# Performance work log

Measured on AMD Instinct MI355X. Metric: run time of the kernel, lower is better.

The kernel has to match this reference:

```python
import jax, jax.numpy as jnp
import numpy as np

N_NODES = 100000
N_EDGES = 1600000
HIDDEN = 128
HALF = HIDDEN // 2
LN_EPS = 1e-5


def setup_inputs() -> dict:
    key = jax.random.key(0)
    ks = jax.random.split(key, 8)
    pos = jax.random.normal(ks[0], (N_NODES, 3), dtype=jnp.float32) * 10.0
    edge_index = jax.random.randint(ks[1], (2, N_EDGES), 0, N_NODES, dtype=jnp.int64)
    batch = jnp.zeros((N_NODES,), dtype=jnp.int64)
    # spatial_encoder params: Linear(3, HALF) -> LayerNorm(HALF) -> GELU -> Linear(HALF, HALF)
    W1 = jax.random.normal(ks[2], (3, HALF), dtype=jnp.float32) * 0.3
    b1 = jax.random.normal(ks[3], (HALF,), dtype=jnp.float32) * 0.05
    ln_g = jnp.ones((HALF,), dtype=jnp.float32)
    ln_b = jnp.zeros((HALF,), dtype=jnp.float32)
    W2 = jax.random.normal(ks[4], (HALF, HALF), dtype=jnp.float32) * 0.1
    b2 = jax.random.normal(ks[5], (HALF,), dtype=jnp.float32) * 0.05
    return {"pos": pos, "edge_index": edge_index, "batch": batch,
            "W1": W1, "b1": b1, "ln_g": ln_g, "ln_b": ln_b, "W2": W2, "b2": b2}


def _layernorm(x, g, b):
    mu = jnp.mean(x, axis=-1, keepdims=True)
    var = jnp.mean((x - mu) ** 2, axis=-1, keepdims=True)
    return (x - mu) * jax.lax.rsqrt(var + LN_EPS) * g + b


def reference(pos, edge_index, batch, W1, b1, ln_g, ln_b, W2, b2):
    num_nodes = pos.shape[0]
    src, dst = edge_index[0], edge_index[1]
    rel = pos[dst] - pos[src]                              # [E, 3]
    dist = jnp.linalg.norm(rel, axis=1, keepdims=True)     # [E, 1]
    rel_n = rel / (dist + 1e-6)
    h = rel_n @ W1 + b1                                    # [E, HALF]
    h = _layernorm(h, ln_g, ln_b)
    h = jax.nn.gelu(h, approximate=False)                  # torch exact GELU
    code = h @ W2 + b2                                     # dropout is identity in eval
    agg = jax.ops.segment_sum(code, dst, num_segments=num_nodes)          # [N, HALF]
    deg = jax.ops.segment_sum(jnp.ones_like(dst, dtype=code.dtype), dst,
                              num_segments=num_nodes)
    deg = jnp.clip(deg, 1.0)
    agg = agg / deg[:, None]
    # original buffer is [N, HIDDEN]; only the first HALF channels receive updates
    out = jnp.concatenate([agg, jnp.zeros_like(agg)], axis=1)             # [N, HIDDEN]
    return out
```

## Files before the change

### kernel.cpp

```cpp
#include <hip/hip_runtime.h>
#include <math.h>

#define HALF 64
#define LN_EPS 1e-5f
#define TCAP 1024
#define TSTR 16

#define GC0 -2.3022082f
#define GC1 -0.1029438f

typedef float f32x2 __attribute__((ext_vector_type(2)));

__device__ __forceinline__ f32x2 pk_fma(f32x2 a, f32x2 b, f32x2 c) {
    f32x2 d;
    asm("v_pk_fma_f32 %0, %1, %2, %3" : "=v"(d) : "v"(a), "v"(b), "v"(c));
    return d;
}
__device__ __forceinline__ f32x2 pk_mul(f32x2 a, f32x2 b) {
    f32x2 d;
    asm("v_pk_mul_f32 %0, %1, %2" : "=v"(d) : "v"(a), "v"(b));
    return d;
}

__device__ __forceinline__ float gelu_fast(float x) {
    const float x2 = x * x;
    const float z  = x * fmaf(GC1, x2, GC0);
    const float e  = __builtin_amdgcn_exp2f(z);
    const float sg = __builtin_amdgcn_rcpf(1.0f + e);
    return x * sg;
}

__global__ void __launch_bounds__(256, 4) bin_kernel(
    const int* __restrict__ ei, int* __restrict__ tcount,
    unsigned* __restrict__ tbuf,
    const float* __restrict__ W1, const float* __restrict__ b1,
    float* __restrict__ fp, int E)
{
    if (blockIdx.x == 0 && threadIdx.x < 64) {
        const int t = threadIdx.x;
        const float w0 = W1[t], w1 = W1[HALF + t], w2 = W1[2 * HALF + t], bb = b1[t];
        float v[14] = { w0, w1, w2, bb,
                        w0 * w0, w0 * w1, w0 * w2, w1 * w1, w1 * w2, w2 * w2,
                        w0 * bb, w1 * bb, w2 * bb, bb * bb };
#pragma unroll
        for (int j = 0; j < 14; ++j) {
            float s = v[j];
#pragma unroll
            for (int off = 32; off; off >>= 1) s += __shfl_down(s, off, 64);
            if (t == 0) fp[j] = s * (1.0f / 64.0f);
        }
    }

    const int e4 = (blockIdx.x * 256 + threadIdx.x) * 4;
    if (e4 >= E) return;
    if (e4 + 3 < E) {
        const int4 s = *(const int4*)(ei + e4);
        const int4 d = *(const int4*)(ei + E + e4);
        const int t0 = d.x >> 4, t1 = d.y >> 4, t2 = d.z >> 4, t3 = d.w >> 4;
        const int s0 = atomicAdd(&tcount[t0 * TSTR], 1);
        const int s1 = atomicAdd(&tcount[t1 * TSTR], 1);
        const int s2 = atomicAdd(&tcount[t2 * TSTR], 1);
        const int s3 = atomicAdd(&tcount[t3 * TSTR], 1);
        if (s0 < TCAP) tbuf[(size_t)t0 * TCAP + s0] = ((unsigned)s.x << 4) | (d.x & 15);
        if (s1 < TCAP) tbuf[(size_t)t1 * TCAP + s1] = ((unsigned)s.y << 4) | (d.y & 15);
        if (s2 < TCAP) tbuf[(size_t)t2 * TCAP + s2] = ((unsigned)s.z << 4) | (d.z & 15);
        if (s3 < TCAP) tbuf[(size_t)t3 * TCAP + s3] = ((unsigned)s.w << 4) | (d.w & 15);
    } else {
        for (int e = e4; e < E; ++e) {
            const int d = ei[E + e];
            const int t = d >> 4;
            const int sl = atomicAdd(&tcount[t * TSTR], 1);
            if (sl < TCAP) tbuf[(size_t)t * TCAP + sl] = ((unsigned)ei[e] << 4) | (d & 15);
        }
    }
}

__global__ void __launch_bounds__(256, 4) nodeout_kernel(
    const unsigned* __restrict__ tbuf,
    const int* __restrict__ tcount,
    const float* __restrict__ pos,
    const float* __restrict__ W1, const float* __restrict__ b1,
    const float* __restrict__ ln_g, const float* __restrict__ ln_b,
    const float* __restrict__ W2, const float* __restrict__ b2,
    const float* __restrict__ fp,
    float* __restrict__ out, int N)
{
    __shared__ unsigned sEdge[TCAP];
    __shared__ float sRx[TCAP + 8];
    __shared__ float sRy[TCAP + 8];
    __shared__ float sRz[TCAP + 8];
    __shared__ float sRw[TCAP + 8];
    __shared__ float sh[16 * 64];
    __shared__ float4 sPd[16];
    __shared__ int   lcnt[16], lofs[16], lcur[16];

    const int tid = threadIdx.x;
    const int lane = tid & 63, w = tid >> 6;
    const int tile = blockIdx.x;
    const int base = tile * 16;

    if (tid < 16) {
        lcnt[tid] = 0;
        const int n = base + tid;
        if (n < N)
            sPd[tid] = make_float4(pos[3 * n], pos[3 * n + 1], pos[3 * n + 2], 0.0f);
    }
    int cnt = tcount[tile * TSTR];
    cnt = (cnt < TCAP) ? cnt : TCAP;

    const float gl = ln_g[lane];
    const float C0 = gl * (W1[lane]            - fp[0]);
    const float C1 = gl * (W1[HALF + lane]     - fp[1]);
    const float C2 = gl * (W1[2 * HALF + lane] - fp[2]);
    const float C3 = gl * (b1[lane]            - fp[3]);
    const float Bl = ln_b[lane];
    const float b2l = b2[lane];
    const f32x2 C0p = { C0, C0 }, C1p = { C1, C1 };
    const f32x2 C2p = { C2, C2 }, C3p = { C3, C3 };
    const f32x2 Blp = { Bl, Bl };
    const f32x2 GC0p = { GC0, GC0 }, GC1p = { GC1, GC1 };

    const float ux = fp[0], uy = fp[1], uz = fp[2], cc = fp[3];
    const float Gxx = fp[4], Gxy = fp[5], Gxz = fp[6];
    const float Gyy = fp[7], Gyz = fp[8], Gzz = fp[9];
    const float px = fp[10], py = fp[11], pz = fp[12], q13 = fp[13];

    __syncthreads();

    const size_t tb = (size_t)tile * TCAP;
    for (int i = tid; i < cnt; i += 256) {
        const unsigned v = tbuf[tb + i];
        sEdge[i] = v;
        atomicAdd(&lcnt[v & 15], 1);
    }
    __syncthreads();

    if (tid < 16) {
        const int v = lcnt[tid];
        int inc = v;
#pragma unroll
        for (int off = 1; off < 16; off <<= 1) {
            const int u = __shfl_up(inc, off, 64);
            if (tid >= off) inc += u;
        }
        lofs[tid] = inc - v;
        lcur[tid] = inc - v;
    }
    __syncthreads();

    for (int i = tid; i < cnt; i += 256) {
        const unsigned v = sEdge[i];
        const int s  = (int)(v >> 4);
        const int dl = (int)(v & 15);
        const float4 pd = sPd[dl];
        const float rx0 = pd.x - pos[3 * s];
        const float ry0 = pd.y - pos[3 * s + 1];
        const float rz0 = pd.z - pos[3 * s + 2];
        const float dist = sqrtf(rx0 * rx0 + ry0 * ry0 + rz0 * rz0);
        const float invd = 1.0f / (dist + 1e-6f);
        const float rx = rx0 * invd, ry = ry0 * invd, rz = rz0 * invd;
        const float mu  = fmaf(ux, rx, fmaf(uy, ry, fmaf(uz, rz, cc)));
        const float ev2 = Gxx * rx * rx + Gyy * ry * ry + Gzz * rz * rz
                        + 2.0f * (Gxy * rx * ry + Gxz * rx * rz
                                  + Gyz * ry * rz + px * rx + py * ry
                                  + pz * rz) + q13;
        const float rstd = rsqrtf(ev2 - mu * mu + LN_EPS);
        const int slot = atomicAdd(&lcur[dl], 1);
        sRx[slot] = rx * rstd;
        sRy[slot] = ry * rstd;
        sRz[slot] = rz * rstd;
        sRw[slot] = rstd;
    }
    __syncthreads();

    const int n0 = base + w * 4;
    const int c0 = lcnt[w * 4 + 0], b0 = lofs[w * 4 + 0];
    const int c1 = lcnt[w * 4 + 1], b1o = lofs[w * 4 + 1];
    const int c2 = lcnt[w * 4 + 2], b2o = lofs[w * 4 + 2];
    const int c3 = lcnt[w * 4 + 3], b3o = lofs[w * 4 + 3];

#define PAIR_LD(V, ARR, IDX)                                                \
        f32x2 V; V.x = ARR[(IDX)]; V.y = ARR[(IDX) + 1];
#define PAIR_GELU(RXP, RYP, RZP, RWP, GA, GB)                               \
        {                                                                   \
            const f32x2 X = pk_fma(C0p, RXP, pk_fma(C1p, RYP,               \
                              pk_fma(C2p, RZP, pk_fma(C3p, RWP, Blp))));    \
            const f32x2 x2 = pk_mul(X, X);                                  \
            const f32x2 zt = pk_fma(GC1p, x2, GC0p);                        \
            const f32x2 z  = pk_mul(X, zt);                                 \
            const float e0 = __builtin_amdgcn_exp2f(z.x);                   \
            const float e1 = __builtin_amdgcn_exp2f(z.y);                   \
            const float r0 = __builtin_amdgcn_rcpf(1.0f + e0);              \
            const float r1 = __builtin_amdgcn_rcpf(1.0f + e1);              \
            GA += X.x * r0;                                                 \
            GB += X.y * r1;                                                 \
        }

#define NODE_ACC(BO, CQ, ROW)                                               \
    {                                                                       \
        const int cntn = (CQ);                                              \
        const int bo = (BO);                                                \
        float accA = 0.0f, accB = 0.0f;                                     \
        int i = 0;                                                          \
        for (; i + 4 <= cntn; i += 4) {                                     \
            PAIR_LD(rx0, sRx, bo + i) PAIR_LD(rx1, sRx, bo + i + 2)         \
            PAIR_LD(ry0, sRy, bo + i) PAIR_LD(ry1, sRy, bo + i + 2)         \
            PAIR_LD(rz0, sRz, bo + i) PAIR_LD(rz1, sRz, bo + i + 2)         \
            PAIR_LD(rw0, sRw, bo + i) PAIR_LD(rw1, sRw, bo + i + 2)         \
            PAIR_GELU(rx0, ry0, rz0, rw0, accA, accB)                       \
            PAIR_GELU(rx1, ry1, rz1, rw1, accA, accB)                       \
        }                                                                   \
        for (; i < cntn; ++i) {                                             \
            const float x = fmaf(C0, sRx[bo + i], fmaf(C1, sRy[bo + i],     \
                              fmaf(C2, sRz[bo + i],                         \
                                   fmaf(C3, sRw[bo + i], Bl))));            \
            accA += gelu_fast(x);                                           \
        }                                                                   \
        sh[(ROW) * 64 + lane] = (cntn > 0)                                  \
            ? (accA + accB) * (1.0f / (float)cntn) : 0.0f;                  \
    }

    NODE_ACC(b0,  c0, w * 4 + 0)
    NODE_ACC(b1o, c1, w * 4 + 1)
    NODE_ACC(b2o, c2, w * 4 + 2)
    NODE_ACC(b3o, c3, w * 4 + 3)
#undef NODE_ACC
#undef PAIR_GELU
#undef PAIR_LD

    __builtin_amdgcn_sched_barrier(0);

    f32x2 wpk[32];
#pragma unroll
    for (int k = 0; k < 32; ++k) {
        wpk[k].x = W2[(2 * k)     * HALF + lane];
        wpk[k].y = W2[(2 * k + 1) * HALF + lane];
    }

#define PHASE2(Q, CQ)                                                       \
    if (n0 + (Q) < N) {                                                     \
        const float* row = sh + (w * 4 + (Q)) * 64;                         \
        f32x2 acc = { 0.0f, 0.0f };                                         \
        _Pragma("unroll")                                                   \
        for (int k = 0; k < 32; ++k) {                                      \
            f32x2 h; h.x = row[2 * k]; h.y = row[2 * k + 1];                \
            acc = pk_fma(h, wpk[k], acc);                                   \
        }                                                                   \
        const float res = ((CQ) > 0) ? (acc.x + acc.y) + b2l : 0.0f;        \
        float* orow = out + (size_t)(n0 + (Q)) * (2 * HALF);                \
        orow[lane] = res;                                                   \
        orow[HALF + lane] = 0.0f;                                           \
    }

    PHASE2(0, c0)
    PHASE2(1, c1)
    PHASE2(2, c2)
    PHASE2(3, c3)
#undef PHASE2
}

extern "C" void kernel_launch(void* const* d_in, const int* in_sizes, int n_in,
                              void* d_out, int out_size, void* d_ws, size_t ws_size,
                              hipStream_t stream) {
    const float* pos = (const float*)d_in[0];
    const int*   ei  = (const int*)d_in[1];
    const float* W1  = (const float*)d_in[3];
    const float* b1  = (const float*)d_in[4];
    const float* g   = (const float*)d_in[5];
    const float* b   = (const float*)d_in[6];
    const float* W2  = (const float*)d_in[7];
    const float* b2  = (const float*)d_in[8];
    float* out = (float*)d_out;

    const int N = in_sizes[0] / 3;
    const int E = in_sizes[1] / 2;
    const int ntile = (N + 15) / 16;

    unsigned* tbuf = (unsigned*)d_ws;
    int* tcount    = (int*)(tbuf + (size_t)ntile * TCAP);
    float* fparams = (float*)(tcount + (size_t)ntile * TSTR);

    const int eb4 = (E / 4 + 255) / 256;

    hipMemsetAsync(tcount, 0, (size_t)ntile * TSTR * sizeof(int), stream);
    bin_kernel<<<eb4, 256, 0, stream>>>(ei, tcount, tbuf, W1, b1, fparams, E);
    nodeout_kernel<<<ntile, 256, 0, stream>>>(tbuf, tcount, pos, W1, b1, g, b,
                                              W2, b2, fparams, out, N);
}
```

Measured before the change: 240.5 us.

## Partition edge bins into eight per-XCD replicas to cut atomic contention

Each tile's edge counter and bucket are replicated eight ways, indexed by blockIdx&7, with per-partition capacity 128. Since blocks are dispatched round-robin across XCDs, each replica is mostly touched by one XCD, reducing cross-die contention and serialization on the counter atomics. The node kernel reads the eight counts, prefix-sums them, and gathers edges from the eight sub-buckets. In exchange the counter memset grows eightfold, the gathers become more scattered, and a skewed partition can now overflow its smaller cap and drop edges.

New measurement: 222.6 us, median of 2. -7.4%, faster.

```diff
diff --git a/kernel.cpp b/kernel.cpp
--- a/kernel.cpp
+++ b/kernel.cpp
@@ -4,6 +4,7 @@
 #define HALF 64
 #define LN_EPS 1e-5f
 #define TCAP 1024
+#define PCAP 128
 #define TSTR 16
 
 #define GC0 -2.3022082f
@@ -34,7 +35,7 @@
     const int* __restrict__ ei, int* __restrict__ tcount,
     unsigned* __restrict__ tbuf,
     const float* __restrict__ W1, const float* __restrict__ b1,
-    float* __restrict__ fp, int E)
+    float* __restrict__ fp, int E, int ntile)
 {
     if (blockIdx.x == 0 && threadIdx.x < 64) {
         const int t = threadIdx.x;
@@ -51,26 +52,33 @@
         }
     }
 
+    const int p = blockIdx.x & 7;
     const int e4 = (blockIdx.x * 256 + threadIdx.x) * 4;
     if (e4 >= E) return;
     if (e4 + 3 < E) {
         const int4 s = *(const int4*)(ei + e4);
         const int4 d = *(const int4*)(ei + E + e4);
         const int t0 = d.x >> 4, t1 = d.y >> 4, t2 = d.z >> 4, t3 = d.w >> 4;
-        const int s0 = atomicAdd(&tcount[t0 * TSTR], 1);
-        const int s1 = atomicAdd(&tcount[t1 * TSTR], 1);
-        const int s2 = atomicAdd(&tcount[t2 * TSTR], 1);
-        const int s3 = atomicAdd(&tcount[t3 * TSTR], 1);
-        if (s0 < TCAP) tbuf[(size_t)t0 * TCAP + s0] = ((unsigned)s.x << 4) | (d.x & 15);
-        if (s1 < TCAP) tbuf[(size_t)t1 * TCAP + s1] = ((unsigned)s.y << 4) | (d.y & 15);
-        if (s2 < TCAP) tbuf[(size_t)t2 * TCAP + s2] = ((unsigned)s.z << 4) | (d.z & 15);
-        if (s3 < TCAP) tbuf[(size_t)t3 * TCAP + s3] = ((unsigned)s.w << 4) | (d.w & 15);
+        const int s0 = atomicAdd(&tcount[((size_t)p * ntile + t0) * TSTR], 1);
+        const int s1 = atomicAdd(&tcount[((size_t)p * ntile + t1) * TSTR], 1);
+        const int s2 = atomicAdd(&tcount[((size_t)p * ntile + t2) * TSTR], 1);
+        const int s3 = atomicAdd(&tcount[((size_t)p * ntile + t3) * TSTR], 1);
+        if (s0 < PCAP)
+            tbuf[((size_t)p * ntile + t0) * PCAP + s0] = ((unsigned)s.x << 4) | (d.x & 15);
+        if (s1 < PCAP)
+            tbuf[((size_t)p * ntile + t1) * PCAP + s1] = ((unsigned)s.y << 4) | (d.y & 15);
+        if (s2 < PCAP)
+            tbuf[((size_t)p * ntile + t2) * PCAP + s2] = ((unsigned)s.z << 4) | (d.z & 15);
+        if (s3 < PCAP)
+            tbuf[((size_t)p * ntile + t3) * PCAP + s3] = ((unsigned)s.w << 4) | (d.w & 15);
     } else {
         for (int e = e4; e < E; ++e) {
             const int d = ei[E + e];
             const int t = d >> 4;
-            const int sl = atomicAdd(&tcount[t * TSTR], 1);
-            if (sl < TCAP) tbuf[(size_t)t * TCAP + sl] = ((unsigned)ei[e] << 4) | (d & 15);
+            const int sl = atomicAdd(&tcount[((size_t)p * ntile + t) * TSTR], 1);
+            if (sl < PCAP)
+                tbuf[((size_t)p * ntile + t) * PCAP + sl] =
+                    ((unsigned)ei[e] << 4) | (d & 15);
         }
     }
 }
@@ -83,7 +91,7 @@
     const float* __restrict__ ln_g, const float* __restrict__ ln_b,
     const float* __restrict__ W2, const float* __restrict__ b2,
     const float* __restrict__ fp,
-    float* __restrict__ out, int N)
+    float* __restrict__ out, int N, int ntile)
 {
     __shared__ unsigned sEdge[TCAP];
     __shared__ float sRx[TCAP + 8];
@@ -93,6 +101,7 @@
     __shared__ float sh[16 * 64];
     __shared__ float4 sPd[16];
     __shared__ int   lcnt[16], lofs[16], lcur[16];
+    __shared__ int   pOff[9];
 
     const int tid = threadIdx.x;
     const int lane = tid & 63, w = tid >> 6;
@@ -105,8 +114,18 @@
         if (n < N)
             sPd[tid] = make_float4(pos[3 * n], pos[3 * n + 1], pos[3 * n + 2], 0.0f);
     }
-    int cnt = tcount[tile * TSTR];
-    cnt = (cnt < TCAP) ? cnt : TCAP;
+    if (tid < 8) {
+        int c = tcount[((size_t)tid * ntile + tile) * TSTR];
+        c = (c < PCAP) ? c : PCAP;
+        int inc = c;
+#pragma unroll
+        for (int off = 1; off < 8; off <<= 1) {
+            const int u = __shfl_up(inc, off, 64);
+            if (tid >= off) inc += u;
+        }
+        pOff[tid + 1] = inc;
+        if (tid == 0) pOff[0] = 0;
+    }
 
     const float gl = ln_g[lane];
     const float C0 = gl * (W1[lane]            - fp[0]);
@@ -126,11 +145,14 @@
     const float px = fp[10], py = fp[11], pz = fp[12], q13 = fp[13];
 
     __syncthreads();
-
-    const size_t tb = (size_t)tile * TCAP;
-    for (int i = tid; i < cnt; i += 256) {
-        const unsigned v = tbuf[tb + i];
-        sEdge[i] = v;
+    const int cnt = pOff[8];
+
+    for (int j = tid; j < cnt; j += 256) {
+        int p = 0;
+#pragma unroll
+        for (int k = 1; k < 8; ++k) p += (j >= pOff[k]) ? 1 : 0;
+        const unsigned v = tbuf[((size_t)p * ntile + tile) * PCAP + (j - pOff[p])];
+        sEdge[j] = v;
         atomicAdd(&lcnt[v & 15], 1);
     }
     __syncthreads();
@@ -277,13 +299,14 @@
     const int ntile = (N + 15) / 16;
 
     unsigned* tbuf = (unsigned*)d_ws;
-    int* tcount    = (int*)(tbuf + (size_t)ntile * TCAP);
-    float* fparams = (float*)(tcount + (size_t)ntile * TSTR);
+    int* tcount    = (int*)(tbuf + (size_t)8 * ntile * PCAP);
+    float* fparams = (float*)(tcount + (size_t)8 * ntile * TSTR);
 
     const int eb4 = (E / 4 + 255) / 256;
 
-    hipMemsetAsync(tcount, 0, (size_t)ntile * TSTR * sizeof(int), stream);
-    bin_kernel<<<eb4, 256, 0, stream>>>(ei, tcount, tbuf, W1, b1, fparams, E);
+    hipMemsetAsync(tcount, 0, (size_t)8 * ntile * TSTR * sizeof(int), stream);
+    bin_kernel<<<eb4, 256, 0, stream>>>(ei, tcount, tbuf, W1, b1, fparams,
+                                        E, ntile);
     nodeout_kernel<<<ntile, 256, 0, stream>>>(tbuf, tcount, pos, W1, b1, g, b,
-                                              W2, b2, fparams, out, N);
-}
+                                              W2, b2, fparams, out, N, ntile);
+}
```
